# Performance work log

Measured on AMD Instinct MI355X. Metric: run time of the kernel, lower is better.

The kernel has to match this reference:

```python
import jax, jax.numpy as jnp
import numpy as np

B, H, S, D = 4, 16, 2048, 64
TEMPERATURE = float(np.sqrt(D))  # 8.0
NEG_INF = -1000000000.0


def setup_inputs() -> dict:
    key = jax.random.key(0)
    kq, kk, kv = jax.random.split(key, 3)
    q = jax.random.normal(kq, (B, H, S, D), dtype=jnp.float32)
    k = jax.random.normal(kk, (B, H, S, D), dtype=jnp.float32)
    v = jax.random.normal(kv, (B, H, S, D), dtype=jnp.float32)
    # causal mask, broadcast over batch and heads: [1,1,S,S], 1 = keep, 0 = masked
    mask = jnp.tril(jnp.ones((S, S), dtype=jnp.int32))[None, None, :, :]
    return {"q": q, "k": k, "v": v, "mask": mask}


def reference(q, k, v, mask):
    # attn = (q / temperature) @ k^T  -> [B,H,S,S]
    attn = jnp.einsum("bhqd,bhkd->bhqk", q / TEMPERATURE, k)
    attn = jnp.where(mask == 0, NEG_INF, attn)
    attn = jax.nn.softmax(attn, axis=-1)  # row-wise over keys
    # dropout is eval-mode (p effectively 0) in this reference
    output = jnp.einsum("bhqk,bhkd->bhqd", attn, v)
    return (output, attn)
```

## Files before the change

### kernel.cpp

```cpp
#include <hip/hip_runtime.h>

#define S_LEN 2048
#define D_DIM 64
#define BQ 128
#define BK 64
#define LDP 72
#define LDPV 68
#define NTHREADS 256

typedef short short8 __attribute__((ext_vector_type(8)));
typedef float float4v __attribute__((ext_vector_type(4)));
typedef unsigned int uint2v __attribute__((ext_vector_type(2)));

__device__ __forceinline__ short f2bf(float f) {
  unsigned int u = __float_as_uint(f);
  u = (u + 0x7FFFu + ((u >> 16) & 1u)) >> 16;
  return (short)u;
}
__device__ __forceinline__ unsigned int pkbf(float a, float b) {
  return (unsigned int)(unsigned short)f2bf(a) |
         ((unsigned int)(unsigned short)f2bf(b) << 16);
}
__device__ __forceinline__ short8 pack8(float4v a, float4v b) {
  short8 r;
  r[0] = f2bf(a.x); r[1] = f2bf(a.y); r[2] = f2bf(a.z); r[3] = f2bf(a.w);
  r[4] = f2bf(b.x); r[5] = f2bf(b.y); r[6] = f2bf(b.z); r[7] = f2bf(b.w);
  return r;
}

__global__ void __launch_bounds__(NTHREADS, 3)
attn_fused(const float* __restrict__ Q, const float* __restrict__ K,
           const float* __restrict__ V, float* __restrict__ Out,
           float* __restrict__ Attn) {
  const int tid  = threadIdx.x;
  const int wave = tid >> 6;
  const int lane = tid & 63;
  const int quad = lane >> 4;
  const int ln16 = lane & 15;
  const int bh   = blockIdx.y;
  const int q0   = blockIdx.x * BQ;
  const int n_kt = (q0 + BQ) >> 6;

  const float* Qp = Q + (size_t)bh * S_LEN * D_DIM;
  const float* Kp = K + (size_t)bh * S_LEN * D_DIM;
  const float* Vp = V + (size_t)bh * S_LEN * D_DIM;
  float* Op = Out  + (size_t)bh * S_LEN * D_DIM;
  float* Ap = Attn + (size_t)bh * S_LEN * S_LEN;

  __shared__ short QP[BQ * LDP];
  __shared__ short Ks[BK * LDP];
  __shared__ short VTs[D_DIM * LDPV];

  {
    const int row = tid >> 1;
    const int h   = (tid & 1) << 5;
    const float* src = Qp + (size_t)(q0 + row) * D_DIM + h;
    float4v q4[8];
#pragma unroll
    for (int i = 0; i < 8; ++i) q4[i] = *(const float4v*)(src + 4 * i);
#pragma unroll
    for (int i = 0; i < 8; ++i) q4[i] *= 0.125f;
    short* dst = &QP[row * LDP + h];
    *(short8*)(dst)      = pack8(q4[0], q4[1]);
    *(short8*)(dst + 8)  = pack8(q4[2], q4[3]);
    *(short8*)(dst + 16) = pack8(q4[4], q4[5]);
    *(short8*)(dst + 24) = pack8(q4[6], q4[7]);
  }
  __syncthreads();

  short8 qf[2][2];
#pragma unroll
  for (int rt = 0; rt < 2; ++rt)
#pragma unroll
    for (int h = 0; h < 2; ++h)
      qf[rt][h] = *(const short8*)&QP[(32 * wave + 16 * rt + ln16) * LDP + 32 * h + quad * 8];

  {
    const int zstart = n_kt * BK;
    if (zstart < S_LEN) {
      const int w4 = (S_LEN - zstart) >> 2;
      float4v z = {0.f, 0.f, 0.f, 0.f};
      for (int row = 0; row < BQ; ++row) {
        float* rp = Ap + (size_t)(q0 + row) * S_LEN + zstart;
        for (int c = tid; c < w4; c += NTHREADS)
          __builtin_nontemporal_store(z, (float4v*)(rp + (c << 2)));
      }
    }
  }

  const int srow = tid >> 2;
  const int sco  = (tid & 3) << 4;
  const int kg   = tid >> 4;
  const int dvg  = tid & 15;

  float l_r[2] = {0.f, 0.f};
  float4v kpre[4];
#pragma unroll
  for (int i = 0; i < 4; ++i)
    kpre[i] = *(const float4v*)(Kp + (size_t)srow * D_DIM + sco + 4 * i);

  for (int kt = 0; kt < n_kt; ++kt) {
    const int k0 = kt << 6;
    __syncthreads();
    {
      short* kd = &Ks[srow * LDP + sco];
      *(short8*)(kd)     = pack8(kpre[0], kpre[1]);
      *(short8*)(kd + 8) = pack8(kpre[2], kpre[3]);
    }
    if (kt + 1 < n_kt) {
      const float* src = Kp + (size_t)(k0 + 64 + srow) * D_DIM + sco;
#pragma unroll
      for (int i = 0; i < 4; ++i) kpre[i] = *(const float4v*)(src + 4 * i);
    }
    __syncthreads();
    const bool diag = (kt >= n_kt - 2);
#pragma unroll
    for (int rt = 0; rt < 2; ++rt) {
      const int qr = q0 + 32 * wave + 16 * rt + ln16;
      float sum = 0.f;
#pragma unroll
      for (int ct = 0; ct < 4; ++ct) {
        const short* kb = &Ks[(16 * ct + ln16) * LDP + quad * 8];
        const short8 b0 = *(const short8*)(kb);
        const short8 b1 = *(const short8*)(kb + 32);
        float4v acc = {0.f, 0.f, 0.f, 0.f};
        acc = __builtin_amdgcn_mfma_f32_16x16x32_bf16(b0, qf[rt][0], acc, 0, 0, 0);
        acc = __builtin_amdgcn_mfma_f32_16x16x32_bf16(b1, qf[rt][1], acc, 0, 0, 0);
#pragma unroll
        for (int reg = 0; reg < 4; ++reg) {
          float e = __expf(acc[reg]);
          if (diag) {
            const int k = k0 + 16 * ct + quad * 4 + reg;
            e = (k > qr) ? 0.f : e;
          }
          sum += e;
        }
      }
      sum += __shfl_xor(sum, 16);
      sum += __shfl_xor(sum, 32);
      l_r[rt] += sum;
    }
  }

  float inv_r[2];
  inv_r[0] = 1.0f / l_r[0];
  inv_r[1] = 1.0f / l_r[1];

  float4v oacc[2][4];
#pragma unroll
  for (int rt = 0; rt < 2; ++rt)
#pragma unroll
    for (int cn = 0; cn < 4; ++cn) oacc[rt][cn] = (float4v){0.f, 0.f, 0.f, 0.f};

  float4v vpre[4];
#pragma unroll
  for (int i = 0; i < 4; ++i)
    kpre[i] = *(const float4v*)(Kp + (size_t)srow * D_DIM + sco + 4 * i);
#pragma unroll
  for (int r = 0; r < 4; ++r)
    vpre[r] = *(const float4v*)(Vp + (size_t)(kg * 4 + r) * D_DIM + dvg * 4);

  for (int kt = 0; kt < n_kt; ++kt) {
    const int k0 = kt << 6;
    __syncthreads();
    {
      short* kd = &Ks[srow * LDP + sco];
      *(short8*)(kd)     = pack8(kpre[0], kpre[1]);
      *(short8*)(kd + 8) = pack8(kpre[2], kpre[3]);
    }
#pragma unroll
    for (int dv = 0; dv < 4; ++dv) {
      uint2v w;
      w.x = pkbf(vpre[0][dv], vpre[1][dv]);
      w.y = pkbf(vpre[2][dv], vpre[3][dv]);
      *(uint2v*)&VTs[(dvg * 4 + dv) * LDPV + kg * 4] = w;
    }
    if (kt + 1 < n_kt) {
      const float* ksrc = Kp + (size_t)(k0 + 64 + srow) * D_DIM + sco;
      const float* vsrc = Vp + (size_t)(k0 + 64 + kg * 4) * D_DIM + dvg * 4;
#pragma unroll
      for (int i = 0; i < 4; ++i) kpre[i] = *(const float4v*)(ksrc + 4 * i);
#pragma unroll
      for (int r = 0; r < 4; ++r) vpre[r] = *(const float4v*)(vsrc + (size_t)r * D_DIM);
    }
    __syncthreads();
    const bool diag = (kt >= n_kt - 2);

#pragma unroll
    for (int rt = 0; rt < 2; ++rt) {
      const int qr   = q0 + 32 * wave + 16 * rt + ln16;
      const int lrow = 32 * wave + 16 * rt + ln16;
      float* arow = Ap + (size_t)qr * S_LEN + k0;
      const float inv = inv_r[rt];
#pragma unroll
      for (int ct = 0; ct < 4; ++ct) {
        const short* kb = &Ks[(16 * ct + ln16) * LDP + quad * 8];
        const short8 b0 = *(const short8*)(kb);
        const short8 b1 = *(const short8*)(kb + 32);
        float4v acc = {0.f, 0.f, 0.f, 0.f};
        acc = __builtin_amdgcn_mfma_f32_16x16x32_bf16(b0, qf[rt][0], acc, 0, 0, 0);
        acc = __builtin_amdgcn_mfma_f32_16x16x32_bf16(b1, qf[rt][1], acc, 0, 0, 0);
        float4v p4;
#pragma unroll
        for (int reg = 0; reg < 4; ++reg) {
          float e = __expf(acc[reg]);
          if (diag) {
            const int k = k0 + 16 * ct + quad * 4 + reg;
            e = (k > qr) ? 0.f : e;
          }
          p4[reg] = e * inv;
        }
        __builtin_nontemporal_store(p4, (float4v*)(arow + 16 * ct + quad * 4));
        uint2v w;
        w.x = pkbf(p4[0], p4[1]);
        w.y = pkbf(p4[2], p4[3]);
        *(uint2v*)&QP[lrow * LDP + 16 * ct + quad * 4] = w;
      }
    }

#pragma unroll
    for (int ks = 0; ks < 2; ++ks) {
#pragma unroll
      for (int rt = 0; rt < 2; ++rt) {
        const short8 aP = *(const short8*)&QP[(32 * wave + 16 * rt + ln16) * LDP + ks * 32 + quad * 8];
#pragma unroll
        for (int cn = 0; cn < 4; ++cn) {
          const short8 bV = *(const short8*)&VTs[(16 * cn + ln16) * LDPV + ks * 32 + quad * 8];
          oacc[rt][cn] = __builtin_amdgcn_mfma_f32_16x16x32_bf16(aP, bV, oacc[rt][cn], 0, 0, 0);
        }
      }
    }
  }

#pragma unroll
  for (int rt = 0; rt < 2; ++rt) {
    const int growb = q0 + 32 * wave + 16 * rt + quad * 4;
#pragma unroll
    for (int cn = 0; cn < 4; ++cn) {
#pragma unroll
      for (int reg = 0; reg < 4; ++reg) {
        Op[(size_t)(growb + reg) * D_DIM + 16 * cn + ln16] = oacc[rt][cn][reg];
      }
    }
  }
}

extern "C" void kernel_launch(void* const* d_in, const int* in_sizes, int n_in,
                              void* d_out, int out_size, void* d_ws, size_t ws_size,
                              hipStream_t stream) {
  const float* q = (const float*)d_in[0];
  const float* k = (const float*)d_in[1];
  const float* v = (const float*)d_in[2];
  float* out  = (float*)d_out;
  float* attn = out + (size_t)4 * 16 * 2048 * 64;
  dim3 grid(S_LEN / BQ, 4 * 16);
  attn_fused<<<grid, NTHREADS, 0, stream>>>(q, k, v, out, attn);
}
```

Before: 1.347 ms.

## Load K fragments straight from global and keep P in registers for PV MFMA

Drops the shared-memory staging for Q and K. Each lane now loads its bf16 MFMA operand fragments directly from global memory, using a permuted key-row mapping chosen so the QK^T output layout lines up with the A-operand layout of the PV MFMA. This lets the probability tile stay in registers instead of round-tripping through LDS. V^T is double-buffered in shared memory, so each iteration needs only one barrier. Also flattens the grid with a block-to-(bh, q-tile) swizzle and raises launch bounds to 4 blocks per CU, at the cost of redundant K global loads per wave, which now rely on cache.

New measurement: 1.517 ms. +12.6%, slower.

```diff
diff --git a/kernel.cpp b/kernel.cpp
--- a/kernel.cpp
+++ b/kernel.cpp
@@ -4,13 +4,13 @@
 #define D_DIM 64
 #define BQ 128
 #define BK 64
-#define LDP 72
-#define LDPV 68
+#define LDV 68
 #define NTHREADS 256
 
 typedef short short8 __attribute__((ext_vector_type(8)));
 typedef float float4v __attribute__((ext_vector_type(4)));
 typedef unsigned int uint2v __attribute__((ext_vector_type(2)));
+typedef unsigned int uint4v __attribute__((ext_vector_type(4)));
 
 __device__ __forceinline__ short f2bf(float f) {
   unsigned int u = __float_as_uint(f);
@@ -28,7 +28,7 @@
   return r;
 }
 
-__global__ void __launch_bounds__(NTHREADS, 3)
+__global__ void __launch_bounds__(NTHREADS, 4)
 attn_fused(const float* __restrict__ Q, const float* __restrict__ K,
            const float* __restrict__ V, float* __restrict__ Out,
            float* __restrict__ Attn) {
@@ -37,8 +37,10 @@
   const int lane = tid & 63;
   const int quad = lane >> 4;
   const int ln16 = lane & 15;
-  const int bh   = blockIdx.y;
-  const int q0   = blockIdx.x * BQ;
+
+  const int bid = blockIdx.x;
+  const int bh  = ((bid & 7) << 3) | ((bid >> 3) & 7);
+  const int q0  = (bid >> 6) * BQ;
   const int n_kt = (q0 + BQ) >> 6;
 
   const float* Qp = Q + (size_t)bh * S_LEN * D_DIM;
@@ -47,33 +49,22 @@
   float* Op = Out  + (size_t)bh * S_LEN * D_DIM;
   float* Ap = Attn + (size_t)bh * S_LEN * S_LEN;
 
-  __shared__ short QP[BQ * LDP];
-  __shared__ short Ks[BK * LDP];
-  __shared__ short VTs[D_DIM * LDPV];
-
-  {
-    const int row = tid >> 1;
-    const int h   = (tid & 1) << 5;
-    const float* src = Qp + (size_t)(q0 + row) * D_DIM + h;
-    float4v q4[8];
-#pragma unroll
-    for (int i = 0; i < 8; ++i) q4[i] = *(const float4v*)(src + 4 * i);
-#pragma unroll
-    for (int i = 0; i < 8; ++i) q4[i] *= 0.125f;
-    short* dst = &QP[row * LDP + h];
-    *(short8*)(dst)      = pack8(q4[0], q4[1]);
-    *(short8*)(dst + 8)  = pack8(q4[2], q4[3]);
-    *(short8*)(dst + 16) = pack8(q4[4], q4[5]);
-    *(short8*)(dst + 24) = pack8(q4[6], q4[7]);
-  }
-  __syncthreads();
+  __shared__ short VT[2][D_DIM * LDV];
 
   short8 qf[2][2];
-#pragma unroll
-  for (int rt = 0; rt < 2; ++rt)
-#pragma unroll
-    for (int h = 0; h < 2; ++h)
-      qf[rt][h] = *(const short8*)&QP[(32 * wave + 16 * rt + ln16) * LDP + 32 * h + quad * 8];
+  const int qr0 = q0 + 32 * wave + ln16;
+#pragma unroll
+  for (int rt = 0; rt < 2; ++rt) {
+    const float* src = Qp + (size_t)(qr0 + 16 * rt) * D_DIM + quad * 8;
+#pragma unroll
+    for (int h = 0; h < 2; ++h) {
+      float4v a = *(const float4v*)(src + 32 * h);
+      float4v b = *(const float4v*)(src + 32 * h + 4);
+      a *= 0.125f;
+      b *= 0.125f;
+      qf[rt][h] = pack8(a, b);
+    }
+  }
 
   {
     const int zstart = n_kt * BK;
@@ -88,60 +79,45 @@
     }
   }
 
-  const int srow = tid >> 2;
-  const int sco  = (tid & 3) << 4;
-  const int kg   = tid >> 4;
-  const int dvg  = tid & 15;
+  const int krl = 8 * (ln16 >> 2) + (ln16 & 3);
 
   float l_r[2] = {0.f, 0.f};
-  float4v kpre[4];
-#pragma unroll
-  for (int i = 0; i < 4; ++i)
-    kpre[i] = *(const float4v*)(Kp + (size_t)srow * D_DIM + sco + 4 * i);
-
   for (int kt = 0; kt < n_kt; ++kt) {
     const int k0 = kt << 6;
-    __syncthreads();
-    {
-      short* kd = &Ks[srow * LDP + sco];
-      *(short8*)(kd)     = pack8(kpre[0], kpre[1]);
-      *(short8*)(kd + 8) = pack8(kpre[2], kpre[3]);
-    }
-    if (kt + 1 < n_kt) {
-      const float* src = Kp + (size_t)(k0 + 64 + srow) * D_DIM + sco;
-#pragma unroll
-      for (int i = 0; i < 4; ++i) kpre[i] = *(const float4v*)(src + 4 * i);
-    }
-    __syncthreads();
     const bool diag = (kt >= n_kt - 2);
-#pragma unroll
-    for (int rt = 0; rt < 2; ++rt) {
-      const int qr = q0 + 32 * wave + 16 * rt + ln16;
-      float sum = 0.f;
-#pragma unroll
-      for (int ct = 0; ct < 4; ++ct) {
-        const short* kb = &Ks[(16 * ct + ln16) * LDP + quad * 8];
-        const short8 b0 = *(const short8*)(kb);
-        const short8 b1 = *(const short8*)(kb + 32);
+    float s0 = 0.f, s1 = 0.f;
+#pragma unroll
+    for (int ct = 0; ct < 4; ++ct) {
+      const int koff = ((ct >> 1) << 5) + ((ct & 1) << 2);
+      const float* kr = Kp + (size_t)(k0 + koff + krl) * D_DIM + quad * 8;
+      const float4v x0 = *(const float4v*)(kr);
+      const float4v x1 = *(const float4v*)(kr + 4);
+      const float4v y0 = *(const float4v*)(kr + 32);
+      const float4v y1 = *(const float4v*)(kr + 36);
+      const short8 b0 = pack8(x0, x1);
+      const short8 b1 = pack8(y0, y1);
+      const int cb = k0 + koff + quad * 8;
+#pragma unroll
+      for (int rt = 0; rt < 2; ++rt) {
         float4v acc = {0.f, 0.f, 0.f, 0.f};
         acc = __builtin_amdgcn_mfma_f32_16x16x32_bf16(b0, qf[rt][0], acc, 0, 0, 0);
         acc = __builtin_amdgcn_mfma_f32_16x16x32_bf16(b1, qf[rt][1], acc, 0, 0, 0);
+        const int qr = qr0 + 16 * rt;
+        float part = 0.f;
 #pragma unroll
         for (int reg = 0; reg < 4; ++reg) {
           float e = __expf(acc[reg]);
-          if (diag) {
-            const int k = k0 + 16 * ct + quad * 4 + reg;
-            e = (k > qr) ? 0.f : e;
-          }
-          sum += e;
+          if (diag) e = (cb + reg > qr) ? 0.f : e;
+          part += e;
         }
-      }
-      sum += __shfl_xor(sum, 16);
-      sum += __shfl_xor(sum, 32);
-      l_r[rt] += sum;
-    }
-  }
-
+        if (rt == 0) s0 += part; else s1 += part;
+      }
+    }
+    l_r[0] += s0;
+    l_r[1] += s1;
+  }
+  l_r[0] += __shfl_xor(l_r[0], 16); l_r[0] += __shfl_xor(l_r[0], 32);
+  l_r[1] += __shfl_xor(l_r[1], 16); l_r[1] += __shfl_xor(l_r[1], 32);
   float inv_r[2];
   inv_r[0] = 1.0f / l_r[0];
   inv_r[1] = 1.0f / l_r[1];
@@ -152,69 +128,76 @@
 #pragma unroll
     for (int cn = 0; cn < 4; ++cn) oacc[rt][cn] = (float4v){0.f, 0.f, 0.f, 0.f};
 
+  const int kg  = tid >> 4;
+  const int dvg = tid & 15;
   float4v vpre[4];
-#pragma unroll
-  for (int i = 0; i < 4; ++i)
-    kpre[i] = *(const float4v*)(Kp + (size_t)srow * D_DIM + sco + 4 * i);
 #pragma unroll
   for (int r = 0; r < 4; ++r)
     vpre[r] = *(const float4v*)(Vp + (size_t)(kg * 4 + r) * D_DIM + dvg * 4);
-
+#pragma unroll
+  for (int dv = 0; dv < 4; ++dv) {
+    uint2v w;
+    w.x = pkbf(vpre[0][dv], vpre[1][dv]);
+    w.y = pkbf(vpre[2][dv], vpre[3][dv]);
+    *(uint2v*)&VT[0][(dvg * 4 + dv) * LDV + kg * 4] = w;
+  }
+#pragma unroll
+  for (int r = 0; r < 4; ++r)
+    vpre[r] = *(const float4v*)(Vp + (size_t)(64 + kg * 4 + r) * D_DIM + dvg * 4);
+
+  int cur = 0;
   for (int kt = 0; kt < n_kt; ++kt) {
     const int k0 = kt << 6;
+    const bool diag = (kt >= n_kt - 2);
     __syncthreads();
-    {
-      short* kd = &Ks[srow * LDP + sco];
-      *(short8*)(kd)     = pack8(kpre[0], kpre[1]);
-      *(short8*)(kd + 8) = pack8(kpre[2], kpre[3]);
-    }
-#pragma unroll
-    for (int dv = 0; dv < 4; ++dv) {
-      uint2v w;
-      w.x = pkbf(vpre[0][dv], vpre[1][dv]);
-      w.y = pkbf(vpre[2][dv], vpre[3][dv]);
-      *(uint2v*)&VTs[(dvg * 4 + dv) * LDPV + kg * 4] = w;
-    }
     if (kt + 1 < n_kt) {
-      const float* ksrc = Kp + (size_t)(k0 + 64 + srow) * D_DIM + sco;
-      const float* vsrc = Vp + (size_t)(k0 + 64 + kg * 4) * D_DIM + dvg * 4;
-#pragma unroll
-      for (int i = 0; i < 4; ++i) kpre[i] = *(const float4v*)(ksrc + 4 * i);
-#pragma unroll
-      for (int r = 0; r < 4; ++r) vpre[r] = *(const float4v*)(vsrc + (size_t)r * D_DIM);
-    }
-    __syncthreads();
-    const bool diag = (kt >= n_kt - 2);
-
-#pragma unroll
-    for (int rt = 0; rt < 2; ++rt) {
-      const int qr   = q0 + 32 * wave + 16 * rt + ln16;
-      const int lrow = 32 * wave + 16 * rt + ln16;
-      float* arow = Ap + (size_t)qr * S_LEN + k0;
-      const float inv = inv_r[rt];
-#pragma unroll
-      for (int ct = 0; ct < 4; ++ct) {
-        const short* kb = &Ks[(16 * ct + ln16) * LDP + quad * 8];
-        const short8 b0 = *(const short8*)(kb);
-        const short8 b1 = *(const short8*)(kb + 32);
+#pragma unroll
+      for (int dv = 0; dv < 4; ++dv) {
+        uint2v w;
+        w.x = pkbf(vpre[0][dv], vpre[1][dv]);
+        w.y = pkbf(vpre[2][dv], vpre[3][dv]);
+        *(uint2v*)&VT[cur ^ 1][(dvg * 4 + dv) * LDV + kg * 4] = w;
+      }
+      if (kt + 2 < n_kt) {
+#pragma unroll
+        for (int r = 0; r < 4; ++r)
+          vpre[r] = *(const float4v*)(Vp + (size_t)(k0 + 128 + kg * 4 + r) * D_DIM + dvg * 4);
+      }
+    }
+
+    uint4v pa[2][2];
+#pragma unroll
+    for (int ct = 0; ct < 4; ++ct) {
+      const int koff = ((ct >> 1) << 5) + ((ct & 1) << 2);
+      const float* kr = Kp + (size_t)(k0 + koff + krl) * D_DIM + quad * 8;
+      const float4v x0 = *(const float4v*)(kr);
+      const float4v x1 = *(const float4v*)(kr + 4);
+      const float4v y0 = *(const float4v*)(kr + 32);
+      const float4v y1 = *(const float4v*)(kr + 36);
+      const short8 b0 = pack8(x0, x1);
+      const short8 b1 = pack8(y0, y1);
+      const int cb = k0 + koff + quad * 8;
+#pragma unroll
+      for (int rt = 0; rt < 2; ++rt) {
         float4v acc = {0.f, 0.f, 0.f, 0.f};
         acc = __builtin_amdgcn_mfma_f32_16x16x32_bf16(b0, qf[rt][0], acc, 0, 0, 0);
         acc = __builtin_amdgcn_mfma_f32_16x16x32_bf16(b1, qf[rt][1], acc, 0, 0, 0);
+        const int qr = qr0 + 16 * rt;
+        const float inv = inv_r[rt];
         float4v p4;
 #pragma unroll
         for (int reg = 0; reg < 4; ++reg) {
           float e = __expf(acc[reg]);
-          if (diag) {
-            const int k = k0 + 16 * ct + quad * 4 + reg;
-            e = (k > qr) ? 0.f : e;
-          }
+          if (diag) e = (cb + reg > qr) ? 0.f : e;
           p4[reg] = e * inv;
         }
-        __builtin_nontemporal_store(p4, (float4v*)(arow + 16 * ct + quad * 4));
-        uint2v w;
-        w.x = pkbf(p4[0], p4[1]);
-        w.y = pkbf(p4[2], p4[3]);
-        *(uint2v*)&QP[lrow * LDP + 16 * ct + quad * 4] = w;
+        __builtin_nontemporal_store(p4, (float4v*)(Ap + (size_t)qr * S_LEN + cb));
+        const unsigned lo = pkbf(p4[0], p4[1]);
+        const unsigned hi = pkbf(p4[2], p4[3]);
+        if (ct == 0)      { pa[rt][0].x = lo; pa[rt][0].y = hi; }
+        else if (ct == 1) { pa[rt][0].z = lo; pa[rt][0].w = hi; }
+        else if (ct == 2) { pa[rt][1].x = lo; pa[rt][1].y = hi; }
+        else              { pa[rt][1].z = lo; pa[rt][1].w = hi; }
       }
     }
 
@@ -222,14 +205,15 @@
     for (int ks = 0; ks < 2; ++ks) {
 #pragma unroll
       for (int rt = 0; rt < 2; ++rt) {
-        const short8 aP = *(const short8*)&QP[(32 * wave + 16 * rt + ln16) * LDP + ks * 32 + quad * 8];
+        const short8 aP = __builtin_bit_cast(short8, pa[rt][ks]);
 #pragma unroll
         for (int cn = 0; cn < 4; ++cn) {
-          const short8 bV = *(const short8*)&VTs[(16 * cn + ln16) * LDPV + ks * 32 + quad * 8];
+          const short8 bV = *(const short8*)&VT[cur][(16 * cn + ln16) * LDV + ks * 32 + quad * 8];
           oacc[rt][cn] = __builtin_amdgcn_mfma_f32_16x16x32_bf16(aP, bV, oacc[rt][cn], 0, 0, 0);
         }
       }
     }
+    cur ^= 1;
   }
 
 #pragma unroll
@@ -253,6 +237,6 @@
   const float* v = (const float*)d_in[2];
   float* out  = (float*)d_out;
   float* attn = out + (size_t)4 * 16 * 2048 * 64;
-  dim3 grid(S_LEN / BQ, 4 * 16);
+  dim3 grid((S_LEN / BQ) * 4 * 16);
   attn_fused<<<grid, NTHREADS, 0, stream>>>(q, k, v, out, attn);
 }
```
